# Kernel optimization log

Hardware: AMD Instinct MI355X
Metric: run time of the kernel (lower is better)

## Reference

```python
import jax, jax.numpy as jnp
from jax import lax
import numpy as np

B, T, F = 32, 512, 512
NUM_OUTPUTS = 23   # joints
DEV_CLASSES = 8
# layer specs: (input_dim, units)
LAYERS = [(F, 1024), (1024, 128), (128, NUM_OUTPUTS),
          (128 + NUM_OUTPUTS, 256), (256, 128), (128, DEV_CLASSES)]


def _gru_params(key, fan_in, units):
    k1, k2, k3 = jax.random.split(key, 3)
    kernel = jax.random.normal(k1, (fan_in, 3 * units), jnp.float32) / jnp.sqrt(jnp.float32(fan_in))
    rkernel = jax.random.normal(k2, (units, 3 * units), jnp.float32) * jnp.float32(0.02)
    bias = jnp.zeros((2, 3 * units), jnp.float32)  # [input_bias, recurrent_bias] (reset_after=True)
    return kernel, rkernel, bias


def setup_inputs() -> dict:
    key = jax.random.key(0)
    keys = jax.random.split(key, 7)
    inp = {"x": jax.random.normal(keys[0], (B, T, F), jnp.float32)}
    for i, (fi, u) in enumerate(LAYERS):
        k, r, b = _gru_params(keys[i + 1], fi, u)
        inp[f"k{i+1}"] = k
        inp[f"r{i+1}"] = r
        inp[f"b{i+1}"] = b
    return inp


def gru(x, kernel, rkernel, bias, act):
    """Keras GRU, reset_after=True, recurrent_activation=sigmoid, gate order z|r|h.
    x: [B,T,F]; kernel: [F,3U]; rkernel: [U,3U]; bias: [2,3U]. Returns [B,T,U]."""
    units = rkernel.shape[0]
    b_i, b_r = bias[0], bias[1]
    # precompute input projections for all timesteps (one big GEMM)
    xp = jnp.einsum('btf,fg->btg', x, kernel) + b_i  # [B,T,3U]

    def step(h, xt):
        rp = h @ rkernel + b_r                       # [B,3U]
        xz, xr, xh = jnp.split(xt, 3, axis=-1)
        rz, rr, rh = jnp.split(rp, 3, axis=-1)
        z = jax.nn.sigmoid(xz + rz)
        r = jax.nn.sigmoid(xr + rr)
        hh = act(xh + r * rh)                        # reset applied AFTER recurrent matmul
        h_new = z * h + (1.0 - z) * hh
        return h_new, h_new

    h0 = jnp.zeros((x.shape[0], units), x.dtype)
    _, ys = lax.scan(step, h0, jnp.swapaxes(xp, 0, 1))  # scan over time
    return jnp.swapaxes(ys, 0, 1)                        # [B,T,U]


relu = jax.nn.relu
linear = lambda v: v


def reference(x, k1, r1, b1, k2, r2, b2, k3, r3, b3,
              k4, r4, b4, k5, r5, b5, k6, r6, b6):
    z = gru(x, k1, r1, b1, relu)          # tcn_gru1: 1024
    z1 = gru(z, k2, r2, b2, relu)         # tcn_gru2: 128
    ye = gru(z1, k3, r3, b3, linear)      # tcn_dgru: num_outputs
    yc = jnp.concatenate([z1, ye], axis=-1)
    y = gru(yc, k4, r4, b4, relu)         # dev_gru1: 256
    y = gru(y, k5, r5, b5, relu)          # dev_gru2: 128
    yd = gru(y, k6, r6, b6, linear)       # dev_dgru: dev_classes
    return ye, yd
```

## Files before the change

### kernel.cpp

```cpp
#include <hip/hip_runtime.h>
#include <hip/hip_bf16.h>
#include <cstdint>
#include <cstddef>

#define BB 32
#define TT 512

typedef short s8v __attribute__((ext_vector_type(8)));
typedef float f4v __attribute__((ext_vector_type(4)));
typedef unsigned long long u64;
typedef unsigned short u16;
typedef unsigned int u32;

__device__ __forceinline__ short f2b(float x) {
  __hip_bfloat16 h = __float2bfloat16(x);
  return *reinterpret_cast<short*>(&h);
}
__device__ __forceinline__ float b2f(u16 x) {
  __hip_bfloat16 h = *reinterpret_cast<__hip_bfloat16*>(&x);
  return __bfloat162float(h);
}
__device__ __forceinline__ float sigm(float x) { return 1.f / (1.f + __expf(-x)); }

__device__ __forceinline__ f4v load16_sc(const void* p) {
  f4v v;
  asm volatile("global_load_dwordx4 %0, %1, off sc0 sc1" : "=v"(v) : "v"(p));
  return v;
}
__device__ __forceinline__ void vm_wait0() {
  asm volatile("s_waitcnt vmcnt(0)" ::: "memory");
}
__device__ __forceinline__ u32 ldP(const u32* p) {
  return __hip_atomic_load(p, __ATOMIC_RELAXED, __HIP_MEMORY_SCOPE_AGENT);
}
__device__ __forceinline__ void stP(u32* p, u32 v) {
  __hip_atomic_store(p, v, __ATOMIC_RELEASE, __HIP_MEMORY_SCOPE_AGENT);
}
__device__ __forceinline__ void stW(u32* p, u32 v) {
  __hip_atomic_store(p, v, __ATOMIC_RELAXED, __HIP_MEMORY_SCOPE_AGENT);
}
__device__ __forceinline__ u32 ldW(const u32* p) {
  return __hip_atomic_load(p, __ATOMIC_RELAXED, __HIP_MEMORY_SCOPE_AGENT);
}

__device__ __forceinline__ void waitP(u32* flags, int baseA, int na, u32 thA,
                                      int baseB, int nbb, u32 thB,
                                      int baseS, int ns, u32 thS) {
  const int tid = threadIdx.x;
  if (tid < 64) {
    for (;;) {
      int ok = 1;
      if (tid < na) ok = (ldP(&flags[(baseA + tid) * 32]) >= thA) ? 1 : 0;
      else if (tid < na + nbb) ok = (ldP(&flags[(baseB + tid - na) * 32]) >= thB) ? 1 : 0;
      else if (tid < na + nbb + ns) ok = (ldP(&flags[(baseS + tid - na - nbb) * 32]) >= thS) ? 1 : 0;
      if (__all(ok)) break;
      __builtin_amdgcn_s_sleep(1);
    }
  }
  __syncthreads();
}

__global__ __launch_bounds__(256) void cast_bf16(const float* __restrict__ in,
                                                 u16* __restrict__ outp, int n4) {
  int i = blockIdx.x * 256 + threadIdx.x;
  if (i < n4) {
    float4 v = *(const float4*)(in + (size_t)i * 4);
    u16 o[4] = {(u16)f2b(v.x), (u16)f2b(v.y), (u16)f2b(v.z), (u16)f2b(v.w)};
    *(u64*)(outp + (size_t)i * 4) = *(const u64*)o;
  }
}

__global__ __launch_bounds__(256) void prep_frags(const float* __restrict__ src,
                                                  u16* __restrict__ dst,
                                                  int N, int Ksrc, int Ks,
                                                  int JT, int U, int recmode, int total_fid) {
  int t = blockIdx.x * 256 + threadIdx.x;
  int lane = t & 63, fid = t >> 6;
  if (fid >= total_fid) return;
  int l15 = lane & 15, quad = lane >> 4;
  int ks = fid % Ks;
  int n, valid_n;
  if (recmode) {
    int rest = fid / Ks;
    int jt = rest % JT;
    int g = rest / JT;
    int jj = jt * 16 + l15;
    n = g * U + jj;
    valid_n = (jj < U) ? 1 : 0;
  } else {
    int nt = fid / Ks;
    n = nt * 16 + l15;
    valid_n = (n < N) ? 1 : 0;
  }
  u16* o = dst + ((size_t)fid * 64 + lane) * 8;
#pragma unroll
  for (int j = 0; j < 8; ++j) {
    int k = ks * 32 + quad * 8 + j;
    float v = (valid_n && k < Ksrc) ? src[(size_t)k * N + n] : 0.f;
    o[j] = (u16)f2b(v);
  }
}

__global__ __launch_bounds__(256) void prep_comb(const float* __restrict__ Kmat,
                                                 const float* __restrict__ Rmat,
                                                 u16* __restrict__ dst,
                                                 int N, int U, int w1v, int w1p,
                                                 int w2v, int w2p, int Ks, int JT,
                                                 int total_fid) {
  int t = blockIdx.x * 256 + threadIdx.x;
  int lane = t & 63, fid = t >> 6;
  if (fid >= total_fid) return;
  int l15 = lane & 15, quad = lane >> 4;
  int ks = fid % Ks;
  int rest = fid / Ks;
  int jt = rest % JT;
  int g = rest / JT;
  int j = jt * 16 + l15;
  bool jv = (j < U);
  int n = g * U + (jv ? j : 0);
  u16* o = dst + ((size_t)fid * 64 + lane) * 8;
#pragma unroll
  for (int jj = 0; jj < 8; ++jj) {
    int k = ks * 32 + quad * 8 + jj;
    float v = 0.f;
    if (jv) {
      if (k < w1p) {
        if (k < w1v) v = Kmat[(size_t)k * N + n];
      } else if (k < w1p + w2p) {
        int kr = k - w1p;
        if (kr < w2v) v = Kmat[(size_t)(w1v + kr) * N + n];
      } else {
        int rr = k - w1p - w2p;
        if (rr < U) v = Rmat[(size_t)rr * N + n];
      }
    }
    o[jj] = (u16)f2b(v);
  }
}

__global__ __launch_bounds__(256) void gemm_mfma(const u16* __restrict__ A, int strideA, int Kact,
                                                 const u16* __restrict__ Bf,
                                                 const float* __restrict__ bias,
                                                 float* __restrict__ C,
                                                 int N, int Ntiles, int Ks,
                                                 int t0, int tcLog2) {
  __shared__ char sha[16 * 2056];
  const int tid = threadIdx.x;
  const int lane = tid & 63, l15 = lane & 15, quad = lane >> 4, w = tid >> 6;
  const int KS4 = Ks * 8;
  const int rowB = Ks * 64 + 8;
  const int bm = blockIdx.y * 16;

  for (int i = tid; i < 16 * KS4; i += 256) {
    int r = i / KS4, u = i - r * KS4;
    u64 v = 0;
    if (u * 4 < Kact) {
      int rl = bm + r;
      size_t grow;
      if (t0 >= 0) {
        int tcm = (1 << tcLog2) - 1;
        grow = (((size_t)(rl >> tcLog2)) << 9) + t0 + (rl & tcm);
      } else {
        grow = (size_t)rl;
      }
      v = *((const u64*)(A + grow * (size_t)strideA) + u);
    }
    *(u64*)(sha + r * rowB + u * 8) = v;
  }
  __syncthreads();

  f4v acc[4];
  f4v z4 = {0.f, 0.f, 0.f, 0.f};
#pragma unroll
  for (int q = 0; q < 4; ++q) acc[q] = z4;

  const int ntb = blockIdx.x * 16 + w * 4;
  for (int ks = 0; ks < Ks; ++ks) {
    int off = l15 * rowB + ks * 64 + quad * 16;
    s8v a = *(const s8v*)(sha + off);
#pragma unroll
    for (int q = 0; q < 4; ++q) {
      int nt = ntb + q;
      if (nt < Ntiles) {
        s8v b = *(const s8v*)(Bf + (((size_t)nt * Ks + ks) * 64 + lane) * 8);
        acc[q] = __builtin_amdgcn_mfma_f32_16x16x32_bf16(a, b, acc[q], 0, 0, 0);
      }
    }
  }
#pragma unroll
  for (int q = 0; q < 4; ++q) {
    int nt = ntb + q;
    if (nt >= Ntiles) continue;
    int col = nt * 16 + l15;
    if (col < N) {
      float bv = bias[col];
#pragma unroll
      for (int r = 0; r < 4; ++r) {
        int rowl = bm + quad * 4 + r;
        C[(size_t)rowl * N + col] = acc[q][r] + bv;
      }
    }
  }
}

struct GCfg {
  const u16 *s1, *s2;
  const u16* Bf;
  const float* bias;
  u16* ydst;
  float* fdst;
  u16* hglob;
  int w1p, w2p, Upad, U, Ks, ksIn, JT, nb, base, act, wfd;
  int baseA, na, baseB, nbb;
};

#define REDOFF 66048
#define SMEM_BYTES 102912
#define HPOFF 74240

__device__ __attribute__((noinline)) void stage_l1(
    const float* xp, const u16* Bf, const float* brec, u16* hbuf, u16* yout,
    u32* flags, int t0, int tc, char* smem) {
  const int tid = threadIdx.x;
  const int lane = tid & 63, l15 = lane & 15, quad = (lane >> 4) & 3;
  const int w = tid >> 6;
  const int kq = w >> 2;
  const int jt_l = (w >> 1) & 1;
  const int Mt = w & 1;
  const int blk = blockIdx.x;
  const int jt = blk * 2 + jt_l;
  const int j = jt * 16 + l15;
  const int HP = 32 * 1024;
  const bool own = (kq == 0);

  float bz = 0.f, brr = 0.f, bh = 0.f;
  float hprev[4];
  if (own) {
    bz = brec[j]; brr = brec[1024 + j]; bh = brec[2048 + j];
    const u32* hp = (const u32*)(hbuf + (size_t)(t0 & 1) * HP);
#pragma unroll
    for (int r = 0; r < 4; ++r) {
      int b = Mt * 16 + quad * 4 + r;
      u32 wd = ldW(hp + ((b * 1024 + (j & ~1)) >> 1));
      hprev[r] = b2f((j & 1) ? (u16)(wd >> 16) : (u16)(wd & 0xffff));
    }
  }

  for (int tt = 0; tt < tc; ++tt) {
    const int t = t0 + tt;
    waitP(flags, 0, 32, (u32)t, 0, 0, 0, 0, 0, 0);
    float xv[3][4];
    if (own) {
#pragma unroll
      for (int r = 0; r < 4; ++r) {
        int b = Mt * 16 + quad * 4 + r;
        const float* xr_ = xp + ((size_t)b * tc + tt) * 3072;
        xv[0][r] = __builtin_nontemporal_load(xr_ + j);
        xv[1][r] = __builtin_nontemporal_load(xr_ + 1024 + j);
        xv[2][r] = __builtin_nontemporal_load(xr_ + 2048 + j);
      }
    }
    {
      const char* hsrc = (const char*)(hbuf + (size_t)(t & 1) * HP);
      f4v vals[4];
#pragma unroll
      for (int i = 0; i < 4; ++i)
        vals[i] = load16_sc(hsrc + (size_t)(tid + i * 1024) * 16);
      vm_wait0();
#pragma unroll
      for (int i = 0; i < 4; ++i) {
        int g16 = tid + i * 1024;
        *(f4v*)(smem + (g16 >> 7) * 2064 + (g16 & 127) * 16) = vals[i];
      }
    }
    __syncthreads();
    f4v acc[3];
    f4v z4 = {0.f, 0.f, 0.f, 0.f};
#pragma unroll
    for (int g = 0; g < 3; ++g) acc[g] = z4;
#pragma unroll
    for (int i = 0; i < 8; ++i) {
      int ks = kq * 8 + i;
      s8v a = *(const s8v*)(smem + (Mt * 16 + l15) * 2064 + ks * 64 + quad * 16);
#pragma unroll
      for (int g = 0; g < 3; ++g) {
        s8v b = *(const s8v*)(Bf + (((size_t)(g * 64 + jt) * 32 + ks) * 64 + lane) * 8);
        acc[g] = __builtin_amdgcn_mfma_f32_16x16x32_bf16(a, b, acc[g], 0, 0, 0);
      }
    }
    if (!own) {
      int idx = (kq - 1) * 4 + (w & 3);
#pragma unroll
      for (int g = 0; g < 3; ++g)
        *(f4v*)(smem + REDOFF + ((g * 12 + idx) * 64 + lane) * 16) = acc[g];
    }
    __syncthreads();
    if (own) {
#pragma unroll
      for (int g = 0; g < 3; ++g)
#pragma unroll
        for (int kk = 0; kk < 3; ++kk) {
          f4v p = *(const f4v*)(smem + REDOFF + ((g * 12 + kk * 4 + w) * 64 + lane) * 16);
          acc[g] += p;
        }
      u16* hdst = hbuf + (size_t)((t + 1) & 1) * HP;
#pragma unroll
      for (int r = 0; r < 4; ++r) {
        int b = Mt * 16 + quad * 4 + r;
        size_t row = (size_t)b * tc + tt;
        float z = sigm(xv[0][r] + acc[0][r] + bz);
        float rr = sigm(xv[1][r] + acc[1][r] + brr);
        float hh = fmaxf(xv[2][r] + rr * (acc[2][r] + bh), 0.f);
        float hnew = z * hprev[r] + (1.f - z) * hh;
        hprev[r] = hnew;
        float part = __shfl_xor(hnew, 1, 64);
        if ((l15 & 1) == 0) {
          u32 wd = (u32)(u16)f2b(hnew) | ((u32)(u16)f2b(part) << 16);
          stW((u32*)hdst + ((b * 1024 + j) >> 1), wd);
          stW((u32*)yout + ((row * 1024 + j) >> 1), wd);
        }
      }
    }
    __syncthreads();
    if (tid == 0) stP(&flags[blk * 32], (u32)(t + 1));
  }
}

__device__ __attribute__((noinline)) void stage_gen(
    const GCfg& c, int bs, u32* flags, int t0, int tc, int initH, char* smem) {
  const int tid = threadIdx.x;
  const int lane = tid & 63, l15 = lane & 15, quad = (lane >> 4) & 3;
  const int w = tid >> 6;
  const int Kc = c.w1p + c.w2p + c.Upad;
  const int rowA = Kc * 2 + 16;
  const int rowH = c.Upad * 2 + 16;
  char* Ab = smem;
  char* Hp = smem + HPOFF;
  const int HB = 32 * rowH;
  const int uIn = (c.w1p + c.w2p) >> 3;
  const int uH = c.Upad >> 3;
  const int upr = uIn + ((c.nb > 1) ? uH : 0);
  const int total_units = 32 * upr;
  const int u1 = c.w1p >> 3;
  const int U = c.U;
  const int HPstride = 32 * c.Upad;

  const int ntask = c.JT * 2;
  int tcount = 0;
  int tjt[2], tmt[2];
#pragma unroll
  for (int i = 0; i < 2; ++i) {
    int task = w * c.nb + bs + i * 16 * c.nb;
    if (task < ntask) { tjt[tcount] = task >> 1; tmt[tcount] = task & 1; ++tcount; }
  }

  const float* b0 = c.bias;
  const float* b1 = c.bias + 3 * U;
  float bz[2], br_[2], bih[2], brh[2];
  int jl[2];
  bool jv[2];
#pragma unroll
  for (int i = 0; i < 2; ++i) {
    if (i >= tcount) { jv[i] = false; jl[i] = 0; bz[i] = br_[i] = bih[i] = brh[i] = 0.f; continue; }
    int j = tjt[i] * 16 + l15;
    jv[i] = (j < U);
    int jc = jv[i] ? j : 0;
    jl[i] = j;
    bz[i] = b0[jc] + b1[jc];
    br_[i] = b0[U + jc] + b1[U + jc];
    bih[i] = b0[2 * U + jc];
    brh[i] = b1[2 * U + jc];
  }

  if (c.nb == 1) {
    for (int i = tid; i < (2 * HB) >> 2; i += 1024) ((u32*)Hp)[i] = 0;
    __syncthreads();
    if (!initH) {
      for (int i = tid; i < 32 * uH; i += 1024) {
        int m = i / uH, u = i - m * uH;
        *(f4v*)(Hp + (t0 & 1) * HB + m * rowH + u * 16) = *((const f4v*)c.hglob + i);
      }
    }
    __syncthreads();
  }

  float hprev[2][4];
#pragma unroll
  for (int i = 0; i < 2; ++i) {
    if (i >= tcount) continue;
#pragma unroll
    for (int r = 0; r < 4; ++r) {
      int b = tmt[i] * 16 + quad * 4 + r;
      float hv;
      if (c.nb > 1) {
        u32 wd = ldW((const u32*)c.hglob + (((t0 & 1) * HPstride + b * c.Upad + (jl[i] & ~1)) >> 1));
        hv = b2f((jl[i] & 1) ? (u16)(wd >> 16) : (u16)(wd & 0xffff));
      } else {
        hv = b2f(*(const u16*)(Hp + (t0 & 1) * HB + b * rowH + jl[i] * 2));
      }
      hprev[i][r] = jv[i] ? hv : 0.f;
    }
  }

  for (int tt = 0; tt < tc; ++tt) {
    const int t = t0 + tt;
    waitP(flags, c.baseA, c.na, (u32)(t + 1), c.baseB, c.nbb, (u32)(t + 1),
          c.base, (c.nb > 1) ? c.nb : 0, (u32)t);
    {
      f4v vals[5];
      int offs[5];
#pragma unroll
      for (int i = 0; i < 5; ++i) {
        int idx = tid + i * 1024;
        int pidx = (idx < total_units) ? idx : (total_units - 1);
        int m = pidx / upr, u = pidx - m * upr;
        const char* src;
        if (u < u1)
          src = (const char*)c.s1 + ((size_t)(m * tc + tt) * c.w1p + (u << 3)) * 2;
        else if (u < uIn)
          src = (const char*)c.s2 + ((size_t)(m * tc + tt) * c.w2p + ((u - u1) << 3)) * 2;
        else
          src = (const char*)c.hglob + ((size_t)(t & 1) * HPstride + m * c.Upad + ((u - uIn) << 3)) * 2;
        vals[i] = load16_sc(src);
        offs[i] = m * rowA + u * 16;
      }
      vm_wait0();
#pragma unroll
      for (int i = 0; i < 5; ++i)
        if (tid + i * 1024 < total_units) *(f4v*)(Ab + offs[i]) = vals[i];
    }
    __syncthreads();
    f4v az[2], ar[2], axh[2], arh[2];
    f4v z4 = {0.f, 0.f, 0.f, 0.f};
#pragma unroll
    for (int i = 0; i < 2; ++i) { az[i] = z4; ar[i] = z4; axh[i] = z4; arh[i] = z4; }
    for (int ks = 0; ks < c.ksIn; ++ks) {
#pragma unroll
      for (int i = 0; i < 2; ++i) {
        if (i >= tcount) break;
        s8v a = *(const s8v*)(Ab + (tmt[i] * 16 + l15) * rowA + ks * 64 + quad * 16);
        const u16* bb = c.Bf + ((size_t)tjt[i] * c.Ks + ks) * 512 + lane * 8;
        s8v bz_ = *(const s8v*)(bb);
        s8v br2 = *(const s8v*)(bb + (size_t)c.JT * c.Ks * 512);
        s8v bh2 = *(const s8v*)(bb + (size_t)2 * c.JT * c.Ks * 512);
        az[i] = __builtin_amdgcn_mfma_f32_16x16x32_bf16(a, bz_, az[i], 0, 0, 0);
        ar[i] = __builtin_amdgcn_mfma_f32_16x16x32_bf16(a, br2, ar[i], 0, 0, 0);
        axh[i] = __builtin_amdgcn_mfma_f32_16x16x32_bf16(a, bh2, axh[i], 0, 0, 0);
      }
    }
    for (int ks = c.ksIn; ks < c.Ks; ++ks) {
#pragma unroll
      for (int i = 0; i < 2; ++i) {
        if (i >= tcount) break;
        s8v a;
        if (c.nb > 1)
          a = *(const s8v*)(Ab + (tmt[i] * 16 + l15) * rowA + ks * 64 + quad * 16);
        else
          a = *(const s8v*)(Hp + (t & 1) * HB + (tmt[i] * 16 + l15) * rowH + (ks - c.ksIn) * 64 + quad * 16);
        const u16* bb = c.Bf + ((size_t)tjt[i] * c.Ks + ks) * 512 + lane * 8;
        s8v bz_ = *(const s8v*)(bb);
        s8v br2 = *(const s8v*)(bb + (size_t)c.JT * c.Ks * 512);
        s8v bh2 = *(const s8v*)(bb + (size_t)2 * c.JT * c.Ks * 512);
        az[i] = __builtin_amdgcn_mfma_f32_16x16x32_bf16(a, bz_, az[i], 0, 0, 0);
        ar[i] = __builtin_amdgcn_mfma_f32_16x16x32_bf16(a, br2, ar[i], 0, 0, 0);
        arh[i] = __builtin_amdgcn_mfma_f32_16x16x32_bf16(a, bh2, arh[i], 0, 0, 0);
      }
    }
#pragma unroll
    for (int i = 0; i < 2; ++i) {
      if (i >= tcount) break;
#pragma unroll
      for (int r = 0; r < 4; ++r) {
        int b = tmt[i] * 16 + quad * 4 + r;
        size_t row = (size_t)b * tc + tt;
        float z = sigm(az[i][r] + bz[i]);
        float rg = sigm(ar[i][r] + br_[i]);
        float hh = axh[i][r] + bih[i] + rg * (arh[i][r] + brh[i]);
        if (c.act) hh = fmaxf(hh, 0.f);
        float hnew = z * hprev[i][r] + (1.f - z) * hh;
        if (!jv[i]) hnew = 0.f;
        hprev[i][r] = hnew;
        int j = jl[i];
        float part = __shfl_xor(hnew, 1, 64);
        u32 wd = (u32)(u16)f2b(hnew) | ((u32)(u16)f2b(part) << 16);
        if ((l15 & 1) == 0) {
          if (c.ydst) stW((u32*)c.ydst + ((row * c.Upad + j) >> 1), wd);
          if (c.nb > 1)
            stW((u32*)c.hglob + ((((t + 1) & 1) * HPstride + b * c.Upad + j) >> 1), wd);
        }
        if (c.nb == 1) *(u16*)(Hp + ((t + 1) & 1) * HB + b * rowH + j * 2) = (u16)f2b(hnew);
        if (c.fdst && jv[i] && j < c.wfd)
          c.fdst[((size_t)b * TT + t) * c.wfd + j] = hnew;
      }
    }
    __syncthreads();
    if (tid == 0) stP(&flags[(c.base + bs) * 32], (u32)(t + 1));
  }
  if (c.nb == 1) {
    int pf = (t0 + tc) & 1;
    for (int i = tid; i < 32 * uH; i += 1024) {
      int m = i / uH, u = i - m * uH;
      *((f4v*)c.hglob + i) = *(const f4v*)(Hp + pf * HB + m * rowH + u * 16);
    }
  }
}

__global__ __launch_bounds__(1024, 1) void pipeline(
    const float* xp, const u16* BfL1, const float* brecL1, u16* hbufL1, u16* y1c,
    GCfg c1, GCfg c2, GCfg c3, GCfg c4, GCfg c5,
    u32* flags, int t0, int tc, int initH) {
  __shared__ char smem[SMEM_BYTES];
  int blk = blockIdx.x;
  if (blk < 32) stage_l1(xp, BfL1, brecL1, hbufL1, y1c, flags, t0, tc, smem);
  else if (blk < 40) stage_gen(c1, blk - 32, flags, t0, tc, initH, smem);
  else if (blk < 41) stage_gen(c2, 0, flags, t0, tc, initH, smem);
  else if (blk < 49) stage_gen(c3, blk - 41, flags, t0, tc, initH, smem);
  else if (blk < 53) stage_gen(c4, blk - 49, flags, t0, tc, initH, smem);
  else stage_gen(c5, 0, flags, t0, tc, initH, smem);
}

extern "C" void kernel_launch(void* const* d_in, const int* in_sizes, int n_in,
                              void* d_out, int out_size, void* d_ws, size_t ws_size,
                              hipStream_t stream) {
  const float* x = (const float*)d_in[0];

  int tcLog2 = 6;
  {
    size_t fixed = (size_t)16384 * 512 * 2
                   + (3145728ull + 1572864ull + 442368 + 15360 + 319488 + 147456 + 7680) * 2
                   + 300000;
    for (; tcLog2 >= 4; --tcLog2) {
      size_t rc = (size_t)BB << tcLog2;
      size_t per = rc * 3072 * 4 + rc * (1024 + 128 + 32 + 256 + 128) * 2 + 8192;
      if (fixed + per <= ws_size || tcLog2 == 4) break;
    }
  }
  const int Tc = 1 << tcLog2;
  const int NCk = TT / Tc;
  const size_t RC = (size_t)BB * Tc;

  char* ws = (char*)d_ws;
  size_t off = 0;
  auto alloc = [&](size_t bytes) -> char* {
    char* p = ws + off;
    off += (bytes + 255) & ~(size_t)255;
    return p;
  };

  u32* flags = (u32*)alloc(54 * 32 * sizeof(u32));
  u16* hbufL1 = (u16*)alloc((size_t)2 * 32 * 1024 * 2);
  u16* hb2 = (u16*)alloc((size_t)2 * 32 * 128 * 2);
  u16* hb4 = (u16*)alloc((size_t)2 * 32 * 256 * 2);
  u16* hb5 = (u16*)alloc((size_t)2 * 32 * 128 * 2);
  u16* hs3 = (u16*)alloc((size_t)32 * 32 * 2);
  u16* hs6 = (u16*)alloc((size_t)32 * 32 * 2);
  u16* recB1 = (u16*)alloc(3145728ull * 2);
  u16* gemB1 = (u16*)alloc(1572864ull * 2);
  u16* cB[5];
  const size_t cBe[5] = {442368, 15360, 319488, 147456, 7680};
  for (int i = 0; i < 5; ++i) cB[i] = (u16*)alloc(cBe[i] * 2);
  u16* x16 = (u16*)alloc((size_t)16384 * 512 * 2);
  float* xp = (float*)alloc(RC * 3072 * sizeof(float));
  u16* y1c = (u16*)alloc(RC * 1024 * 2);
  u16* y2c = (u16*)alloc(RC * 128 * 2);
  u16* yec = (u16*)alloc(RC * 32 * 2);
  u16* y4c = (u16*)alloc(RC * 256 * 2);
  u16* y5c = (u16*)alloc(RC * 128 * 2);

  float* outye = (float*)d_out;
  float* outyd = outye + (size_t)BB * TT * 23;

  hipMemsetAsync(flags, 0, 54 * 32 * sizeof(u32), stream);
  hipMemsetAsync(hbufL1, 0, (size_t)2 * 32 * 1024 * 2, stream);
  hipMemsetAsync(hb2, 0, (size_t)2 * 32 * 128 * 2, stream);
  hipMemsetAsync(hb4, 0, (size_t)2 * 32 * 256 * 2, stream);
  hipMemsetAsync(hb5, 0, (size_t)2 * 32 * 128 * 2, stream);

  {
    int n4 = (16384 * 512) / 4;
    hipLaunchKernelGGL(cast_bf16, dim3((n4 + 255) / 256), dim3(256), 0, stream, x, x16, n4);
    hipLaunchKernelGGL(prep_frags, dim3((3 * 64 * 32 * 64 + 255) / 256), dim3(256), 0, stream,
                       (const float*)d_in[2], recB1, 3072, 1024, 32, 64, 1024, 1, 3 * 64 * 32);
    hipLaunchKernelGGL(prep_frags, dim3((192 * 16 * 64 + 255) / 256), dim3(256), 0, stream,
                       (const float*)d_in[1], gemB1, 3072, 512, 16, 0, 0, 0, 192 * 16);
    const int pc[5][8] = {
        {384, 128, 1024, 1024, 0, 0, 36, 8},
        {69, 23, 128, 128, 0, 0, 5, 2},
        {768, 256, 128, 128, 23, 32, 13, 16},
        {384, 128, 256, 256, 0, 0, 12, 8},
        {24, 8, 128, 128, 0, 0, 5, 1}};
    for (int i = 0; i < 5; ++i) {
      int l = i + 1;
      int tf = 3 * pc[i][7] * pc[i][6];
      hipLaunchKernelGGL(prep_comb, dim3((tf * 64 + 255) / 256), dim3(256), 0, stream,
                         (const float*)d_in[1 + 3 * l], (const float*)d_in[2 + 3 * l], cB[i],
                         pc[i][0], pc[i][1], pc[i][2], pc[i][3], pc[i][4], pc[i][5],
                         pc[i][6], pc[i][7], tf);
    }
  }

  GCfg c1 = {y1c, nullptr, cB[0], (const float*)d_in[6], y2c, nullptr, hb2,
             1024, 0, 128, 128, 36, 32, 8, 8, 32, 1, 0, 0, 32, 0, 0};
  GCfg c2 = {y2c, nullptr, cB[1], (const float*)d_in[9], yec, outye, hs3,
             128, 0, 32, 23, 5, 4, 2, 1, 40, 0, 23, 32, 8, 0, 0};
  GCfg c3 = {y2c, yec, cB[2], (const float*)d_in[12], y4c, nullptr, hb4,
             128, 32, 256, 256, 13, 5, 16, 8, 41, 1, 0, 32, 8, 40, 1};
  GCfg c4 = {y4c, nullptr, cB[3], (const float*)d_in[15], y5c, nullptr, hb5,
             256, 0, 128, 128, 12, 8, 8, 4, 49, 1, 0, 41, 8, 0, 0};
  GCfg c5 = {y5c, nullptr, cB[4], (const float*)d_in[18], nullptr, outyd, hs6,
             128, 0, 32, 8, 5, 4, 1, 1, 53, 0, 8, 49, 4, 0, 0};

  const float* biasL1 = (const float*)d_in[3];

  for (int c = 0; c < NCk; ++c) {
    const int t0 = c * Tc;
    hipLaunchKernelGGL(gemm_mfma, dim3(12, (unsigned)(RC / 16)), dim3(256), 0, stream,
                       x16, 512, 512, gemB1, biasL1, xp, 3072, 192, 16, t0, tcLog2);
    hipLaunchKernelGGL(pipeline, dim3(54), dim3(1024), 0, stream,
                       xp, recB1, biasL1 + 3072, hbufL1, y1c,
                       c1, c2, c3, c4, c5, flags, t0, Tc, (c == 0) ? 1 : 0);
  }
}
```

Before: 14.23 ms.

## Replicate progress flags per consumer block and use relaxed stores

Each producer block now writes its step counter into a separate cache-line slot for every consumer block, so consumers poll private copies instead of all spinning on one shared flag line. The release store becomes a relaxed store, and the L1 stage's h-buffer load is moved ahead of the x projection loads. The aim is to cut contention and latency on the inter-block barrier of this persistent pipeline. In exchange the flag array grows 64-fold and each publish issues many stores; dropping release ordering depends on the preceding __syncthreads and stW stores being visible, which is a memory-ordering risk.

```diff
diff --git a/kernel.cpp b/kernel.cpp
--- a/kernel.cpp
+++ b/kernel.cpp
@@ -33,9 +33,6 @@
 __device__ __forceinline__ u32 ldP(const u32* p) {
   return __hip_atomic_load(p, __ATOMIC_RELAXED, __HIP_MEMORY_SCOPE_AGENT);
 }
-__device__ __forceinline__ void stP(u32* p, u32 v) {
-  __hip_atomic_store(p, v, __ATOMIC_RELEASE, __HIP_MEMORY_SCOPE_AGENT);
-}
 __device__ __forceinline__ void stW(u32* p, u32 v) {
   __hip_atomic_store(p, v, __ATOMIC_RELAXED, __HIP_MEMORY_SCOPE_AGENT);
 }
@@ -47,12 +44,13 @@
                                       int baseB, int nbb, u32 thB,
                                       int baseS, int ns, u32 thS) {
   const int tid = threadIdx.x;
+  const int rep = blockIdx.x;
   if (tid < 64) {
     for (;;) {
       int ok = 1;
-      if (tid < na) ok = (ldP(&flags[(baseA + tid) * 32]) >= thA) ? 1 : 0;
-      else if (tid < na + nbb) ok = (ldP(&flags[(baseB + tid - na) * 32]) >= thB) ? 1 : 0;
-      else if (tid < na + nbb + ns) ok = (ldP(&flags[(baseS + tid - na - nbb) * 32]) >= thS) ? 1 : 0;
+      if (tid < na) ok = (ldP(&flags[((baseA + tid) * 64 + rep) * 32]) >= thA) ? 1 : 0;
+      else if (tid < na + nbb) ok = (ldP(&flags[((baseB + tid - na) * 64 + rep) * 32]) >= thB) ? 1 : 0;
+      else if (tid < na + nbb + ns) ok = (ldP(&flags[((baseS + tid - na - nbb) * 64 + rep) * 32]) >= thS) ? 1 : 0;
       if (__all(ok)) break;
       __builtin_amdgcn_s_sleep(1);
     }
@@ -212,6 +210,7 @@
   u16* hglob;
   int w1p, w2p, Upad, U, Ks, ksIn, JT, nb, base, act, wfd;
   int baseA, na, baseB, nbb;
+  int pubF, pubN;
 };
 
 #define REDOFF 66048
@@ -249,6 +248,20 @@
   for (int tt = 0; tt < tc; ++tt) {
     const int t = t0 + tt;
     waitP(flags, 0, 32, (u32)t, 0, 0, 0, 0, 0, 0);
+    {
+      const char* hsrc = (const char*)(hbuf + (size_t)(t & 1) * HP);
+      f4v vals[4];
+#pragma unroll
+      for (int i = 0; i < 4; ++i)
+        vals[i] = load16_sc(hsrc + (size_t)(tid + i * 1024) * 16);
+      vm_wait0();
+#pragma unroll
+      for (int i = 0; i < 4; ++i) {
+        int g16 = tid + i * 1024;
+        *(f4v*)(smem + (g16 >> 7) * 2064 + (g16 & 127) * 16) = vals[i];
+      }
+    }
+    __syncthreads();
     float xv[3][4];
     if (own) {
 #pragma unroll
@@ -260,20 +273,6 @@
         xv[2][r] = __builtin_nontemporal_load(xr_ + 2048 + j);
       }
     }
-    {
-      const char* hsrc = (const char*)(hbuf + (size_t)(t & 1) * HP);
-      f4v vals[4];
-#pragma unroll
-      for (int i = 0; i < 4; ++i)
-        vals[i] = load16_sc(hsrc + (size_t)(tid + i * 1024) * 16);
-      vm_wait0();
-#pragma unroll
-      for (int i = 0; i < 4; ++i) {
-        int g16 = tid + i * 1024;
-        *(f4v*)(smem + (g16 >> 7) * 2064 + (g16 & 127) * 16) = vals[i];
-      }
-    }
-    __syncthreads();
     f4v acc[3];
     f4v z4 = {0.f, 0.f, 0.f, 0.f};
 #pragma unroll
@@ -322,7 +321,7 @@
       }
     }
     __syncthreads();
-    if (tid == 0) stP(&flags[blk * 32], (u32)(t + 1));
+    if (tid < 40) stW(&flags[(blk * 64 + tid) * 32], (u32)(t + 1));
   }
 }
 
@@ -494,7 +493,8 @@
       }
     }
     __syncthreads();
-    if (tid == 0) stP(&flags[(c.base + bs) * 32], (u32)(t + 1));
+    if (tid < c.pubN)
+      stW(&flags[((c.base + bs) * 64 + c.pubF + tid) * 32], (u32)(t + 1));
   }
   if (c.nb == 1) {
     int pf = (t0 + tc) & 1;
@@ -528,7 +528,7 @@
   {
     size_t fixed = (size_t)16384 * 512 * 2
                    + (3145728ull + 1572864ull + 442368 + 15360 + 319488 + 147456 + 7680) * 2
-                   + 300000;
+                   + 700000;
     for (; tcLog2 >= 4; --tcLog2) {
       size_t rc = (size_t)BB << tcLog2;
       size_t per = rc * 3072 * 4 + rc * (1024 + 128 + 32 + 256 + 128) * 2 + 8192;
@@ -547,7 +547,7 @@
     return p;
   };
 
-  u32* flags = (u32*)alloc(54 * 32 * sizeof(u32));
+  u32* flags = (u32*)alloc((size_t)54 * 64 * 32 * sizeof(u32));
   u16* hbufL1 = (u16*)alloc((size_t)2 * 32 * 1024 * 2);
   u16* hb2 = (u16*)alloc((size_t)2 * 32 * 128 * 2);
   u16* hb4 = (u16*)alloc((size_t)2 * 32 * 256 * 2);
@@ -570,7 +570,7 @@
   float* outye = (float*)d_out;
   float* outyd = outye + (size_t)BB * TT * 23;
 
-  hipMemsetAsync(flags, 0, 54 * 32 * sizeof(u32), stream);
+  hipMemsetAsync(flags, 0, (size_t)54 * 64 * 32 * sizeof(u32), stream);
   hipMemsetAsync(hbufL1, 0, (size_t)2 * 32 * 1024 * 2, stream);
   hipMemsetAsync(hb2, 0, (size_t)2 * 32 * 128 * 2, stream);
   hipMemsetAsync(hb4, 0, (size_t)2 * 32 * 256 * 2, stream);
@@ -600,15 +600,15 @@
   }
 
   GCfg c1 = {y1c, nullptr, cB[0], (const float*)d_in[6], y2c, nullptr, hb2,
-             1024, 0, 128, 128, 36, 32, 8, 8, 32, 1, 0, 0, 32, 0, 0};
+             1024, 0, 128, 128, 36, 32, 8, 8, 32, 1, 0, 0, 32, 0, 0, 32, 17};
   GCfg c2 = {y2c, nullptr, cB[1], (const float*)d_in[9], yec, outye, hs3,
-             128, 0, 32, 23, 5, 4, 2, 1, 40, 0, 23, 32, 8, 0, 0};
+             128, 0, 32, 23, 5, 4, 2, 1, 40, 0, 23, 32, 8, 0, 0, 41, 8};
   GCfg c3 = {y2c, yec, cB[2], (const float*)d_in[12], y4c, nullptr, hb4,
-             128, 32, 256, 256, 13, 5, 16, 8, 41, 1, 0, 32, 8, 40, 1};
+             128, 32, 256, 256, 13, 5, 16, 8, 41, 1, 0, 32, 8, 40, 1, 41, 12};
   GCfg c4 = {y4c, nullptr, cB[3], (const float*)d_in[15], y5c, nullptr, hb5,
-             256, 0, 128, 128, 12, 8, 8, 4, 49, 1, 0, 41, 8, 0, 0};
+             256, 0, 128, 128, 12, 8, 8, 4, 49, 1, 0, 41, 8, 0, 0, 49, 5};
   GCfg c5 = {y5c, nullptr, cB[4], (const float*)d_in[18], nullptr, outyd, hs6,
-             128, 0, 32, 8, 5, 4, 1, 1, 53, 0, 8, 49, 4, 0, 0};
+             128, 0, 32, 8, 5, 4, 1, 1, 53, 0, 8, 49, 4, 0, 0, 0, 0};
 
   const float* biasL1 = (const float*)d_in[3];
 
```

After: 14.18 ms. No clear change (-0.4%).
